# Performance work log

Hardware: AMD Instinct MI355X
Metric: run time of the kernel (lower is better)

Reference implementation:

```python
import jax, jax.numpy as jnp
import numpy as np


def _layernorm(x, g, b, eps=1e-5):
    mu = jnp.mean(x, axis=-1, keepdims=True)
    var = jnp.var(x, axis=-1, keepdims=True)
    return (x - mu) * jax.lax.rsqrt(var + eps) * g + b


def _forward(x_real, x_imag, dt, conv_w, conv_b, spec_re, spec_im, lam_re, lam_im,
             dt_param, sigma, noise_r, noise_i, ln_g, ln_b, W1, b1, w2, b2,
             Jg_W, Jg_b, Rg_W, Rg_b):
    B, T, C, H, W = x_real.shape
    x = x_real + 1j * x_imag  # complex field [B,T,C,H,W]

    # ---- spatial mixer: 3x3 conv applied to real/imag parts (linear op) ----
    def conv(z):
        z2 = z.reshape(B * T, C, H, W)
        y = jax.lax.conv_general_dilated(z2, conv_w, (1, 1), 'SAME',
                                         dimension_numbers=('NCHW', 'OIHW', 'NCHW'))
        return (y + conv_b[None, :, None, None]).reshape(B, T, C, H, W)
    x = x + (conv(x.real) + 1j * conv(x.imag))

    # ---- spectral mixer: pointwise complex filter in FFT domain ----
    Xf = jnp.fft.fft2(x, axes=(-2, -1), norm='ortho')
    filt = (spec_re + 1j * spec_im)[None, None]  # [1,1,C,H,W]
    x = x + jnp.fft.ifft2(Xf * filt, axes=(-2, -1), norm='ortho')

    # ---- metriplectic propagator: diagonal SSM scan in rfft2 space ----
    dt_eff = dt * jax.nn.softplus(dt_param)          # [C]
    dt_scalar = dt_eff.mean()
    xs = jnp.concatenate([x.real, x.imag], axis=0)   # [2B,T,C,H,W]; B_out=2B
    u = jnp.fft.rfft2(xs, axes=(-2, -1), norm='ortho')  # [2B,T,C,H,Wf]
    lam = -jax.nn.softplus(lam_re) + 1j * lam_im     # stable poles, [C]
    A = jnp.exp(lam * dt_eff.astype(jnp.complex64))  # [C]
    A = jnp.broadcast_to(A[None, None, :, None, None], u.shape)

    def comb(e1, e2):  # first-order linear recurrence h_t = a_t h_{t-1} + u_t
        a1, u1 = e1
        a2, u2 = e2
        return (a1 * a2, a2 * u1 + u2)
    _, h = jax.lax.associative_scan(comb, (A, u), axis=1)

    xt = jnp.fft.irfft2(h, s=(H, W), axes=(-2, -1), norm='ortho')  # [2B,T,C,H,W] real
    x_temporal = xt[:B] + 1j * xt[B:]

    noise = (noise_r + 1j * noise_i) * sigma * jnp.sqrt(dt_scalar)
    x = x + x_temporal + noise

    # ---- Port-Hamiltonian layer on real||imag channel concat ----
    xp = jnp.transpose(x, (0, 1, 3, 4, 2))                  # [B,T,H,W,C]
    xc = jnp.concatenate([xp.real, xp.imag], axis=-1)       # [B,T,H,W,2C]
    D = 2 * C
    x_in = _layernorm(xc, ln_g, ln_b)
    # grads of potential H = sum(MLP(x_in)) wrt x_in
    pot = lambda z: (jax.nn.silu(z @ W1 + b1) @ w2 + b2).sum()
    grads = jax.grad(pot)(x_in)
    M = (x_in @ Jg_W + Jg_b).reshape(*xc.shape[:-1], D, D)
    Jm = M - jnp.swapaxes(M, -1, -2)
    P = (x_in @ Rg_W + Rg_b).reshape(*xc.shape[:-1], D, D)
    R = jnp.einsum('...ki,...kj->...ij', P, P) + 1e-4 * jnp.eye(D, dtype=xc.dtype)
    update = jnp.einsum('...ij,...j->...i', Jm - R, grads)
    x_ph = xc + update * dt_scalar

    # output: [B,T,2C,H,W]; real half = out.real, imag half = out.imag
    return jnp.transpose(x_ph, (0, 1, 4, 2, 3))


def setup_inputs() -> dict:
    key = jax.random.key(0)
    ks = jax.random.split(key, 16)
    B, T, C, H, W = 2, 8, 16, 64, 64
    D = 2 * C
    hid = D * 4
    f32 = jnp.float32
    rn = lambda k, s, sc=1.0: jax.random.normal(k, s, f32) * sc
    return dict(
        x_real=rn(ks[0], (B, T, C, H, W)),
        x_imag=rn(ks[1], (B, T, C, H, W)),
        dt=jnp.asarray(0.1, f32),
        conv_w=rn(ks[2], (C, C, 3, 3), 0.05),
        conv_b=jnp.zeros((C,), f32),
        spec_re=rn(ks[3], (C, H, W), 0.1),
        spec_im=rn(ks[4], (C, H, W), 0.1),
        lam_re=rn(ks[5], (C,)),
        lam_im=rn(ks[6], (C,)),
        dt_param=rn(ks[7], (C,)),
        sigma=jnp.asarray(0.01, f32),
        noise_r=rn(ks[8], (B, T, C, H, W)),
        noise_i=rn(ks[9], (B, T, C, H, W)),
        ln_g=jnp.ones((D,), f32),
        ln_b=jnp.zeros((D,), f32),
        W1=rn(ks[10], (D, hid), 0.1),
        b1=jnp.zeros((hid,), f32),
        w2=rn(ks[11], (hid,), 0.1),
        b2=jnp.asarray(0.0, f32),
        Jg_W=rn(ks[12], (D, D * D), 0.02),
        Jg_b=jnp.zeros((D * D,), f32),
        Rg_W=rn(ks[13], (D, D * D), 0.02),
        Rg_b=jnp.zeros((D * D,), f32),
    )


def reference(x_real, x_imag, dt, conv_w, conv_b, spec_re, spec_im, lam_re, lam_im,
              dt_param, sigma, noise_r, noise_i, ln_g, ln_b, W1, b1, w2, b2,
              Jg_W, Jg_b, Rg_W, Rg_b):
    return _forward(x_real, x_imag, dt, conv_w, conv_b, spec_re, spec_im, lam_re,
                    lam_im, dt_param, sigma, noise_r, noise_i, ln_g, ln_b, W1, b1,
                    w2, b2, Jg_W, Jg_b, Rg_W, Rg_b)
```

## Files before the change

kernel.cpp:

```cpp
#include <hip/hip_runtime.h>
#include <math.h>
#include <utility>

#define Bb 2
#define Tt 8
#define Cc 16
#define Hh 64
#define Ww 64
#define Dd 32
#define HID 128
#define NPIX 4096
#define NIMG 256

typedef unsigned short ushort_t;
typedef unsigned int uint_t;
typedef __attribute__((ext_vector_type(8))) short short8;
typedef __attribute__((ext_vector_type(4))) float f32x4;
union U16 { uint4 u; short8 s; };

__device__ __forceinline__ float sp_f(float x) {
    return (x > 20.f) ? x : log1pf(expf(x));
}

__device__ __forceinline__ ushort_t f2bf(float f) {
    uint_t u = __float_as_uint(f);
    uint_t r = (u + 0x7fffu + ((u >> 16) & 1u)) >> 16;
    return (ushort_t)r;
}
__device__ __forceinline__ float bf2f(ushort_t h) { return __uint_as_float(((uint_t)h) << 16); }

__device__ __forceinline__ uint_t packbf(float hi, float lo) {
    return __builtin_amdgcn_perm(__float_as_uint(hi), __float_as_uint(lo), 0x07060302u);
}
__device__ __forceinline__ uint4 synth8(const float* gf, float xs) {
    uint4 r;
    r.x = packbf(gf[1] * xs, gf[0] * xs);
    r.y = packbf(gf[3] * xs, gf[2] * xs);
    r.z = packbf(gf[5] * xs, gf[4] * xs);
    r.w = packbf(gf[7] * xs, gf[6] * xs);
    return r;
}
__device__ __forceinline__ void expand8(uint4 v, float* f) {
    f[0] = __uint_as_float(v.x << 16); f[1] = __uint_as_float(v.x & 0xffff0000u);
    f[2] = __uint_as_float(v.y << 16); f[3] = __uint_as_float(v.y & 0xffff0000u);
    f[4] = __uint_as_float(v.z << 16); f[5] = __uint_as_float(v.z & 0xffff0000u);
    f[6] = __uint_as_float(v.w << 16); f[7] = __uint_as_float(v.w & 0xffff0000u);
}

template <typename F, int... Is>
__device__ __forceinline__ void unroll_impl(F&& f, std::integer_sequence<int, Is...>) {
    (f(std::integral_constant<int, Is>{}), ...);
}
template <int N, typename F>
__device__ __forceinline__ void cunroll(F&& f) {
    unroll_impl(f, std::make_integer_sequence<int, N>{});
}

#define MFMA16(a, b, c) __builtin_amdgcn_mfma_f32_16x16x32_bf16((a), (b), (c), 0, 0, 0)

struct cpx { float r, i; };
__device__ __forceinline__ cpx cadd(cpx a, cpx b) { return {a.r + b.r, a.i + b.i}; }
__device__ __forceinline__ cpx csub(cpx a, cpx b) { return {a.r - b.r, a.i - b.i}; }
__device__ __forceinline__ cpx cmulw(cpx a, float wr, float wi) {
    return {a.r * wr - a.i * wi, a.r * wi + a.i * wr};
}
template<int S>
__device__ __forceinline__ cpx cmulSi(cpx a) {
    return {-(float)S * a.i, (float)S * a.r};
}
template<int S>
__device__ __forceinline__ void dft8(cpx* y) {
    const float C = 0.70710678118654752f;
    cpx t0 = cadd(y[0], y[4]), t1 = csub(y[0], y[4]);
    cpx t2 = cadd(y[2], y[6]), t3 = csub(y[2], y[6]);
    cpx e0 = cadd(t0, t2), e2 = csub(t0, t2);
    cpx t3i = cmulSi<S>(t3);
    cpx e1 = cadd(t1, t3i), e3 = csub(t1, t3i);
    cpx u0 = cadd(y[1], y[5]), u1 = csub(y[1], y[5]);
    cpx u2 = cadd(y[3], y[7]), u3 = csub(y[3], y[7]);
    cpx o0 = cadd(u0, u2), o2 = csub(u0, u2);
    cpx u3i = cmulSi<S>(u3);
    cpx o1 = cadd(u1, u3i), o3 = csub(u1, u3i);
    o1 = cmulw(o1, C, (float)S * C);
    o2 = cmulSi<S>(o2);
    o3 = cmulw(o3, -C, (float)S * C);
    y[0] = cadd(e0, o0); y[4] = csub(e0, o0);
    y[1] = cadd(e1, o1); y[5] = csub(e1, o1);
    y[2] = cadd(e2, o2); y[6] = csub(e2, o2);
    y[3] = cadd(e3, o3); y[7] = csub(e3, o3);
}

template<int S>
__device__ __forceinline__ void fft2d_r8(float* reM, float* imM,
                                         const float* twr, const float* twi, int tid) {
    int j = tid & 63, g = tid >> 6;
    {
        cpx y[8];
        #pragma unroll
        for (int n1 = 0; n1 < 8; ++n1) {
            int a = j * 65 + n1 * 8 + g;
            y[n1] = {reM[a], imM[a]};
        }
        dft8<S>(y);
        #pragma unroll
        for (int k1 = 0; k1 < 8; ++k1) {
            int m = (g * k1) & 63;
            cpx b = cmulw(y[k1], twr[m], twi[m]);
            int a = j * 65 + k1 * 8 + g;
            reM[a] = b.r; imM[a] = b.i;
        }
    }
    __syncthreads();
    {
        cpx y[8];
        #pragma unroll
        for (int n2 = 0; n2 < 8; ++n2) {
            int a = j * 65 + g * 8 + n2;
            y[n2] = {reM[a], imM[a]};
        }
        dft8<S>(y);
        __syncthreads();
        #pragma unroll
        for (int k2 = 0; k2 < 8; ++k2) {
            int a = j * 65 + g + k2 * 8;
            reM[a] = y[k2].r; imM[a] = y[k2].i;
        }
    }
    __syncthreads();
    {
        cpx y[8];
        #pragma unroll
        for (int n1 = 0; n1 < 8; ++n1) {
            int a = (n1 * 8 + g) * 65 + j;
            y[n1] = {reM[a], imM[a]};
        }
        dft8<S>(y);
        #pragma unroll
        for (int k1 = 0; k1 < 8; ++k1) {
            int m = (g * k1) & 63;
            cpx b = cmulw(y[k1], twr[m], twi[m]);
            int a = (k1 * 8 + g) * 65 + j;
            reM[a] = b.r; imM[a] = b.i;
        }
    }
    __syncthreads();
    {
        cpx y[8];
        #pragma unroll
        for (int n2 = 0; n2 < 8; ++n2) {
            int a = (g * 8 + n2) * 65 + j;
            y[n2] = {reM[a], imM[a]};
        }
        dft8<S>(y);
        __syncthreads();
        #pragma unroll
        for (int k2 = 0; k2 < 8; ++k2) {
            int a = (g + k2 * 8) * 65 + j;
            reM[a] = y[k2].r; imM[a] = y[k2].i;
        }
    }
    __syncthreads();
}

__global__ __launch_bounds__(256)
void k_conv(const float* __restrict__ xr, const float* __restrict__ xi,
            const float* __restrict__ cw, const float* __restrict__ cb,
            float2* __restrict__ x1,
            const float* __restrict__ JW, const float* __restrict__ Jb,
            const float* __restrict__ RW, const float* __restrict__ Rb,
            const float* __restrict__ W1, const float* __restrict__ dtp,
            const float* __restrict__ dt_param,
            ushort_t* __restrict__ B1f, ushort_t* __restrict__ B2f,
            ushort_t* __restrict__ w1n, ushort_t* __restrict__ w1t,
            float* __restrict__ dts_out) {
    __shared__ float sre[Cc][18][18];
    __shared__ float sim[Cc][18][18];
    __shared__ float swt[8 * 16 * 12];
    __shared__ float sb[8];
    int tid = threadIdx.x;
    if (blockIdx.x >= 512) {
        const int N1 = 33 * 2048, N2 = 33 * 1024, N3 = 4096;
        int i = (blockIdx.x - 512) * 256 + tid;
        for (; i < N1 + N2 + N3; i += 40 * 256) {
            if (i < N1) {
                int s = i / 2048; int r = i % 2048;
                int ch = r >> 9; int lane = (r >> 3) & 63; int e = i & 7;
                int n = ch * 16 + (lane & 15);
                int k = s * 32 + ((lane >> 4) << 3) + e;
                float v;
                if (k < 1024) {
                    int d = k >> 5, rr = k & 31;
                    if (n < 32) v = JW[d * 1024 + n * 32 + rr] - JW[d * 1024 + rr * 32 + n];
                    else        v = RW[d * 1024 + (n - 32) * 32 + rr];
                } else {
                    int rr = k - 1024;
                    if (n < 32) v = Jb[n * 32 + rr] - Jb[rr * 32 + n];
                    else        v = Rb[(n - 32) * 32 + rr];
                }
                B1f[i] = f2bf(v);
            } else if (i < N1 + N2) {
                int i2 = i - N1;
                int s = i2 / 1024; int r = i2 % 1024;
                int ch = r >> 9; int lane = (r >> 3) & 63; int e = i2 & 7;
                int n = ch * 16 + (lane & 15);
                int k = s * 32 + ((lane >> 4) << 3) + e;
                float v;
                if (k < 1024) {
                    int d = k >> 5, kk = k & 31;
                    v = RW[d * 1024 + kk * 32 + n];
                } else {
                    v = Rb[(k - 1024) * 32 + n];
                }
                B2f[i2] = f2bf(v);
            } else {
                int i3 = i - N1 - N2;
                int d = i3 >> 7, h = i3 & 127;
                ushort_t v = f2bf(W1[i3]);
                w1n[i3] = v;
                w1t[h * 32 + d] = v;
            }
        }
        if (blockIdx.x == 512 && tid == 0) {
            float s = 0.f;
            for (int c = 0; c < Cc; ++c) s += sp_f(dt_param[c]);
            dts_out[0] = dtp[0] * s * (1.f / Cc);
        }
        return;
    }
    int blk = blockIdx.x;
    int bt = blk >> 5;
    int sub = blk & 31;
    int tile = sub >> 1, cohalf = sub & 1;
    int ty0 = (tile >> 2) * 16, tx0 = (tile & 3) * 16;
    for (int i = tid; i < 8 * 16 * 9; i += 256) {
        int g = i / 9, k = i % 9;
        swt[g * 12 + k] = cw[cohalf * 8 * 144 + i];
    }
    if (tid < 8) sb[tid] = cb[cohalf * 8 + tid];
    for (int i = tid; i < Cc * 18 * 18; i += 256) {
        int ci = i / 324; int r = i % 324; int y = r / 18, x = r % 18;
        int gy = ty0 + y - 1, gx = tx0 + x - 1;
        float vr = 0.f, vi = 0.f;
        if (gy >= 0 && gy < Hh && gx >= 0 && gx < Ww) {
            int gidx = (bt * Cc + ci) * NPIX + gy * Ww + gx;
            vr = xr[gidx]; vi = xi[gidx];
        }
        sre[ci][y][x] = vr; sim[ci][y][x] = vi;
    }
    __syncthreads();
    int py = tid >> 4, px = tid & 15;
    int gy = ty0 + py, gx = tx0 + px;
    float ar[8], ai[8];
    #pragma unroll
    for (int oc = 0; oc < 8; ++oc) {
        int cg = cohalf * 8 + oc;
        ar[oc] = sre[cg][py + 1][px + 1] + sb[oc];
        ai[oc] = sim[cg][py + 1][px + 1] + sb[oc];
    }
    for (int ci = 0; ci < Cc; ++ci) {
        float nr[9], ni[9];
        #pragma unroll
        for (int dy = 0; dy < 3; ++dy)
            #pragma unroll
            for (int dx = 0; dx < 3; ++dx) {
                nr[dy * 3 + dx] = sre[ci][py + dy][px + dx];
                ni[dy * 3 + dx] = sim[ci][py + dy][px + dx];
            }
        #pragma unroll
        for (int oc = 0; oc < 8; ++oc) {
            const float* wp = &swt[(oc * 16 + ci) * 12];
            float4 w0 = *(const float4*)&wp[0];
            float4 w1 = *(const float4*)&wp[4];
            float w8 = wp[8];
            ar[oc] += w0.x * nr[0] + w0.y * nr[1] + w0.z * nr[2]
                    + w0.w * nr[3] + w1.x * nr[4] + w1.y * nr[5]
                    + w1.z * nr[6] + w1.w * nr[7] + w8 * nr[8];
            ai[oc] += w0.x * ni[0] + w0.y * ni[1] + w0.z * ni[2]
                    + w0.w * ni[3] + w1.x * ni[4] + w1.y * ni[5]
                    + w1.z * ni[6] + w1.w * ni[7] + w8 * ni[8];
        }
    }
    #pragma unroll
    for (int oc = 0; oc < 8; ++oc)
        x1[(bt * Cc + cohalf * 8 + oc) * NPIX + gy * Ww + gx] = make_float2(ar[oc], ai[oc]);
}

__global__ __launch_bounds__(512)
void k_fft_fwd(const float2* __restrict__ x1,
               const float* __restrict__ spec_re, const float* __restrict__ spec_im,
               float2* __restrict__ X2f) {
    int img = blockIdx.x;
    int c = img % Cc;
    int tid = threadIdx.x;
    __shared__ float re[64 * 65], im[64 * 65];
    __shared__ float twr[64], twi[64];
    if (tid < 64) {
        float ang = -0.098174770424681038798f * (float)tid;
        twr[tid] = cosf(ang); twi[tid] = sinf(ang);
    }
    const float2* src = x1 + (size_t)img * NPIX;
    for (int idx = tid; idx < NPIX; idx += 512) {
        int h = idx >> 6, w = idx & 63;
        float2 v = src[idx];
        re[h * 65 + w] = v.x; im[h * 65 + w] = v.y;
    }
    __syncthreads();
    fft2d_r8<-1>(re, im, twr, twi, tid);
    const float* fr = spec_re + c * NPIX;
    const float* fi = spec_im + c * NPIX;
    float2* dst = X2f + (size_t)img * NPIX;
    for (int idx = tid; idx < NPIX; idx += 512) {
        int h = idx >> 6, w = idx & 63;
        float xr_ = re[h * 65 + w], xi_ = im[h * 65 + w];
        float gr = 1.f + fr[idx], gi = fi[idx];
        dst[idx] = make_float2(xr_ * gr - xi_ * gi, xi_ * gr + xr_ * gi);
    }
}

__global__ __launch_bounds__(256)
void k_scan2(const float2* __restrict__ Z,
             const float* __restrict__ lam_re, const float* __restrict__ lam_im,
             const float* __restrict__ dt_param, const float* __restrict__ dtp,
             float2* __restrict__ S) {
    int id = blockIdx.x * 256 + threadIdx.x;
    int w = id & 63;
    int c = (id >> 12) & 15;
    int b = id >> 16;
    float dte = dtp[0] * sp_f(dt_param[c]);
    float ea = expf(-sp_f(lam_re[c]) * dte);
    float ph = lam_im[c] * dte;
    float Ar = ea * cosf(ph), Ai = ea * sinf(ph);
    if (w > 32) Ai = -Ai;
    bool sc = (w == 0) || (w == 32);
    int pix = id & (NPIX - 1);
    int base = (b * Tt * Cc + c) * NPIX + pix;
    float s1r = 0.f, s1i = 0.f, s2r = 0.f, s2i = 0.f;
    #pragma unroll
    for (int t = 0; t < Tt; ++t) {
        int idx = base + t * (Cc * NPIX);
        float2 zv = Z[idx];
        float nr = Ar * s1r - Ai * s1i + zv.x;
        float ni = Ar * s1i + Ai * s1r + zv.y;
        s1r = nr; s1i = ni;
        float zr, zi;
        if (sc) {
            nr = Ar * s2r + Ai * s2i + zv.x;
            ni = Ar * s2i - Ai * s2r + zv.y;
            s2r = nr; s2i = ni;
            zr = 0.5f * (s1r + s2r); zi = 0.5f * (s1i + s2i);
        } else { zr = s1r; zi = s1i; }
        S[idx] = make_float2(zv.x + zr, zv.y + zi);
    }
}

__global__ __launch_bounds__(512)
void k_fft_inv(const float2* __restrict__ Sp,
               const float* __restrict__ noise_r, const float* __restrict__ noise_i,
               const float* __restrict__ sigma_p, const float* __restrict__ dts_p,
               float2* __restrict__ xf) {
    int img = blockIdx.x; int tid = threadIdx.x;
    __shared__ float re[64 * 65], im[64 * 65];
    __shared__ float twr[64], twi[64];
    if (tid < 64) {
        float ang = 0.098174770424681038798f * (float)tid;
        twr[tid] = cosf(ang); twi[tid] = sinf(ang);
    }
    const float2* src = Sp + (size_t)img * NPIX;
    for (int idx = tid; idx < NPIX; idx += 512) {
        int h = idx >> 6, w = idx & 63;
        float2 v = src[idx];
        re[h * 65 + w] = v.x; im[h * 65 + w] = v.y;
    }
    __syncthreads();
    fft2d_r8<1>(re, im, twr, twi, tid);
    float ns = sigma_p[0] * sqrtf(dts_p[0]);
    const float inv = 1.f / 4096.f;
    float2* dst = xf + (size_t)img * NPIX;
    const float* nr = noise_r + (size_t)img * NPIX;
    const float* ni = noise_i + (size_t)img * NPIX;
    for (int idx = tid; idx < NPIX; idx += 512) {
        int h = idx >> 6, w = idx & 63;
        dst[idx] = make_float2(re[h * 65 + w] * inv + ns * nr[idx],
                               im[h * 65 + w] * inv + ns * ni[idx]);
    }
}

__global__ __launch_bounds__(256, 2)
void k_ph(const float2* __restrict__ field,
          const float* __restrict__ ln_g, const float* __restrict__ ln_b,
          const float* __restrict__ b1, const float* __restrict__ w2,
          const ushort_t* __restrict__ w1n, const ushort_t* __restrict__ w1t,
          const ushort_t* __restrict__ B1f, const ushort_t* __restrict__ B2f,
          const float* __restrict__ dts_p,
          float* __restrict__ out) {
    __shared__ ushort_t xin_s[128 * 40];
    __shared__ ushort_t g_s[128 * 40];
    __shared__ ushort_t pg_s[128 * 40];
    __shared__ ushort_t A_s[128 * 136] __attribute__((aligned(16)));

    int tid = threadIdx.x;
    int bt = blockIdx.x >> 5;
    int pix0 = (blockIdx.x & 31) << 7;

    int p = tid & 127, half = tid >> 7;
    const float2* fbase = field + ((size_t)bt * 16) * NPIX + pix0 + p;
    float2 xv[8];
    float s1 = 0.f, s2 = 0.f;
    #pragma unroll
    for (int j = 0; j < 8; ++j) {
        xv[j] = fbase[(half * 8 + j) * NPIX];
        s1 += xv[j].x + xv[j].y;
        s2 += xv[j].x * xv[j].x + xv[j].y * xv[j].y;
    }
    float2* red = (float2*)A_s;
    red[p * 2 + half] = make_float2(s1, s2);
    __syncthreads();
    float2 r0 = red[p * 2], r1 = red[p * 2 + 1];
    float mu = (r0.x + r1.x) * 0.03125f;
    float var = (r0.y + r1.y) * 0.03125f - mu * mu;
    float rs = rsqrtf(var + 1e-5f);
    #pragma unroll
    for (int j = 0; j < 8; ++j) {
        int cf = half * 8 + j;
        xin_s[p * 40 + cf]      = f2bf((xv[j].x - mu) * rs * ln_g[cf] + ln_b[cf]);
        xin_s[p * 40 + cf + 16] = f2bf((xv[j].y - mu) * rs * ln_g[cf + 16] + ln_b[cf + 16]);
    }
    __syncthreads();

    int lane = tid & 63, wv = tid >> 6;
    int quad = lane >> 4, l15 = lane & 15;
    const f32x4 zero4 = {0.f, 0.f, 0.f, 0.f};
    int m0 = wv * 32;

    f32x4 zacc[2][8];
    #pragma unroll
    for (int mt = 0; mt < 2; ++mt)
        #pragma unroll
        for (int nt = 0; nt < 8; ++nt) zacc[mt][nt] = zero4;
    U16 az[2];
    #pragma unroll
    for (int mt = 0; mt < 2; ++mt)
        az[mt].u = *(const uint4*)&xin_s[(m0 + mt * 16 + l15) * 40 + quad * 8];
    #pragma unroll
    for (int nt = 0; nt < 8; ++nt) {
        U16 bz;
        bz.u = *(const uint4*)&w1t[(nt * 16 + l15) * 32 + quad * 8];
        zacc[0][nt] = MFMA16(az[0].s, bz.s, zacc[0][nt]);
        zacc[1][nt] = MFMA16(az[1].s, bz.s, zacc[1][nt]);
    }
    #pragma unroll
    for (int nt = 0; nt < 8; ++nt) {
        int col = nt * 16 + l15;
        float b1v = b1[col], w2v = w2[col];
        #pragma unroll
        for (int mt = 0; mt < 2; ++mt) {
            #pragma unroll
            for (int r = 0; r < 4; ++r) {
                int row = m0 + mt * 16 + quad * 4 + r;
                float z = zacc[mt][nt][r] + b1v;
                float s = 1.f / (1.f + expf(-z));
                float t = s * (1.f + z * (1.f - s)) * w2v;
                A_s[row * 136 + col] = f2bf(t);
            }
        }
    }
    __syncthreads();

    f32x4 gacc[2][2];
    #pragma unroll
    for (int mt = 0; mt < 2; ++mt)
        #pragma unroll
        for (int nt = 0; nt < 2; ++nt) gacc[mt][nt] = zero4;
    #pragma unroll
    for (int q = 0; q < 4; ++q) {
        U16 ag[2];
        #pragma unroll
        for (int mt = 0; mt < 2; ++mt)
            ag[mt].u = *(const uint4*)&A_s[(m0 + mt * 16 + l15) * 136 + q * 32 + quad * 8];
        #pragma unroll
        for (int nt = 0; nt < 2; ++nt) {
            U16 bg;
            bg.u = *(const uint4*)&w1n[(nt * 16 + l15) * 128 + q * 32 + quad * 8];
            gacc[0][nt] = MFMA16(ag[0].s, bg.s, gacc[0][nt]);
            gacc[1][nt] = MFMA16(ag[1].s, bg.s, gacc[1][nt]);
        }
    }
    #pragma unroll
    for (int mt = 0; mt < 2; ++mt)
        #pragma unroll
        for (int nt = 0; nt < 2; ++nt)
            #pragma unroll
            for (int r = 0; r < 4; ++r)
                g_s[(m0 + mt * 16 + quad * 4 + r) * 40 + nt * 16 + l15] = f2bf(gacc[mt][nt][r]);
    __syncthreads();

    const ushort_t* xr0 = &xin_s[(m0 + l15) * 40];
    const ushort_t* xr1 = &xin_s[(m0 + 16 + l15) * 40];
    uint4 gvp0 = *(const uint4*)&g_s[(m0 + l15) * 40 + quad * 8];
    uint4 gvp1 = *(const uint4*)&g_s[(m0 + 16 + l15) * 40 + quad * 8];
    float gf0[8], gf1[8];
    expand8(gvp0, gf0);
    expand8(gvp1, gf1);
    const uint4* B1v = (const uint4*)B1f;
    const uint4* B2v = (const uint4*)B2f;

    uint4 br[2][4];
    #pragma unroll
    for (int pf = 0; pf < 2; ++pf)
        #pragma unroll
        for (int ch = 0; ch < 4; ++ch)
            br[pf][ch] = B1v[(pf * 4 + ch) * 64 + lane];
    f32x4 acc1[4][2];
    #pragma unroll
    for (int ch = 0; ch < 4; ++ch) { acc1[ch][0] = zero4; acc1[ch][1] = zero4; }
    cunroll<33>([&](auto Sc) {
        constexpr int s = Sc.value;
        constexpr int cur = s & 1;
        U16 a0, a1;
        if constexpr (s < 32) {
            float x0 = bf2f(xr0[s]);
            float x1 = bf2f(xr1[s]);
            a0.u = synth8(gf0, x0);
            a1.u = synth8(gf1, x1);
        } else {
            a0.u = gvp0; a1.u = gvp1;
        }
        #pragma unroll
        for (int ch = 0; ch < 4; ++ch) {
            U16 b; b.u = br[cur][ch];
            acc1[ch][0] = MFMA16(a0.s, b.s, acc1[ch][0]);
            acc1[ch][1] = MFMA16(a1.s, b.s, acc1[ch][1]);
        }
        if constexpr (s + 2 < 33) {
            #pragma unroll
            for (int ch = 0; ch < 4; ++ch)
                br[cur][ch] = B1v[((s + 2) * 4 + ch) * 64 + lane];
        }
    });
    #pragma unroll
    for (int mt = 0; mt < 2; ++mt)
        #pragma unroll
        for (int c2 = 0; c2 < 2; ++c2)
            #pragma unroll
            for (int r = 0; r < 4; ++r)
                pg_s[(m0 + mt * 16 + quad * 4 + r) * 40 + c2 * 16 + l15] =
                    f2bf(acc1[2 + c2][mt][r]);
    __syncthreads();

    uint4 pgp0 = *(const uint4*)&pg_s[(m0 + l15) * 40 + quad * 8];
    uint4 pgp1 = *(const uint4*)&pg_s[(m0 + 16 + l15) * 40 + quad * 8];
    float pgf0[8], pgf1[8];
    expand8(pgp0, pgf0);
    expand8(pgp1, pgf1);
    uint4 br2[2][2];
    #pragma unroll
    for (int pf = 0; pf < 2; ++pf) {
        br2[pf][0] = B2v[(pf * 2 + 0) * 64 + lane];
        br2[pf][1] = B2v[(pf * 2 + 1) * 64 + lane];
    }
    f32x4 acc2[2][2];
    acc2[0][0] = zero4; acc2[0][1] = zero4; acc2[1][0] = zero4; acc2[1][1] = zero4;
    cunroll<33>([&](auto Sc) {
        constexpr int s = Sc.value;
        constexpr int cur = s & 1;
        U16 a0, a1;
        if constexpr (s < 32) {
            float x0 = bf2f(xr0[s]);
            float x1 = bf2f(xr1[s]);
            a0.u = synth8(pgf0, x0);
            a1.u = synth8(pgf1, x1);
        } else {
            a0.u = pgp0; a1.u = pgp1;
        }
        #pragma unroll
        for (int ch = 0; ch < 2; ++ch) {
            U16 b; b.u = br2[cur][ch];
            acc2[ch][0] = MFMA16(a0.s, b.s, acc2[ch][0]);
            acc2[ch][1] = MFMA16(a1.s, b.s, acc2[ch][1]);
        }
        if constexpr (s + 2 < 33) {
            br2[cur][0] = B2v[((s + 2) * 2 + 0) * 64 + lane];
            br2[cur][1] = B2v[((s + 2) * 2 + 1) * 64 + lane];
        }
    });

    __syncthreads();
    float* upd = (float*)A_s;
    #pragma unroll
    for (int mt = 0; mt < 2; ++mt) {
        #pragma unroll
        for (int c2 = 0; c2 < 2; ++c2) {
            int col = c2 * 16 + l15;
            #pragma unroll
            for (int r = 0; r < 4; ++r) {
                int row = m0 + mt * 16 + quad * 4 + r;
                float gval = bf2f(g_s[row * 40 + col]);
                upd[row * 33 + col] = acc1[c2][mt][r] - acc2[c2][mt][r] - 1e-4f * gval;
            }
        }
    }
    __syncthreads();
    float dts = dts_p[0];
    #pragma unroll
    for (int cc = 0; cc < 16; ++cc) {
        int c = half * 16 + cc;
        float2 v = fbase[cc * NPIX];
        float xcv = half ? v.y : v.x;
        out[((size_t)bt * 32 + c) * NPIX + pix0 + p] = xcv + dts * upd[p * 33 + c];
    }
}

extern "C" void kernel_launch(void* const* d_in, const int* in_sizes, int n_in,
                              void* d_out, int out_size, void* d_ws, size_t ws_size,
                              hipStream_t stream) {
    const float* x_real   = (const float*)d_in[0];
    const float* x_imag   = (const float*)d_in[1];
    const float* dt       = (const float*)d_in[2];
    const float* conv_w   = (const float*)d_in[3];
    const float* conv_b   = (const float*)d_in[4];
    const float* spec_re  = (const float*)d_in[5];
    const float* spec_im  = (const float*)d_in[6];
    const float* lam_re   = (const float*)d_in[7];
    const float* lam_im   = (const float*)d_in[8];
    const float* dt_param = (const float*)d_in[9];
    const float* sigma    = (const float*)d_in[10];
    const float* noise_r  = (const float*)d_in[11];
    const float* noise_i  = (const float*)d_in[12];
    const float* ln_g     = (const float*)d_in[13];
    const float* ln_b     = (const float*)d_in[14];
    const float* W1       = (const float*)d_in[15];
    const float* b1       = (const float*)d_in[16];
    const float* w2       = (const float*)d_in[17];
    const float* Jg_W     = (const float*)d_in[19];
    const float* Jg_b     = (const float*)d_in[20];
    const float* Rg_W     = (const float*)d_in[21];
    const float* Rg_b     = (const float*)d_in[22];

    float2* wsA = (float2*)d_ws;
    float2* wsB = wsA + 1048576;
    float2* wsS = wsB + 1048576;

    ushort_t* B1f = (ushort_t*)(wsS + 1048576);
    ushort_t* B2f = B1f + 33 * 2048;
    ushort_t* w1n = B2f + 33 * 1024;
    ushort_t* w1t = w1n + 4096;
    float*    dts = (float*)(w1t + 4096);

    k_conv<<<552, 256, 0, stream>>>(x_real, x_imag, conv_w, conv_b, wsA,
                                    Jg_W, Jg_b, Rg_W, Rg_b, W1, dt, dt_param,
                                    B1f, B2f, w1n, w1t, dts);
    k_fft_fwd<<<NIMG, 512, 0, stream>>>(wsA, spec_re, spec_im, wsB);
    k_scan2<<<512, 256, 0, stream>>>(wsB, lam_re, lam_im, dt_param, dt, wsS);
    k_fft_inv<<<NIMG, 512, 0, stream>>>(wsS, noise_r, noise_i, sigma, dts, wsA);
    k_ph<<<512, 256, 0, stream>>>(wsA, ln_g, ln_b, b1, w2, w1n, w1t, B1f, B2f, dts,
                                  (float*)d_out);
}
```

Before: 182.3 us.

## Fuse temporal scan into inverse FFT kernel via direct convolution over time

Removes the separate scan kernel and its intermediate buffer. Each inverse-FFT block now builds its timestep's scan output directly as a weighted sum of earlier frequency-domain frames, using powers of the pole, before running the inverse FFT. This saves one launch and one full write and read of the intermediate field, but a block at timestep t reads t+1 frames, so total reads rise to roughly 4.5x the field across the blocks.

```diff
diff --git a/kernel.cpp b/kernel.cpp
--- a/kernel.cpp
+++ b/kernel.cpp
@@ -317,59 +317,53 @@
     }
 }
 
-__global__ __launch_bounds__(256)
-void k_scan2(const float2* __restrict__ Z,
-             const float* __restrict__ lam_re, const float* __restrict__ lam_im,
-             const float* __restrict__ dt_param, const float* __restrict__ dtp,
-             float2* __restrict__ S) {
-    int id = blockIdx.x * 256 + threadIdx.x;
-    int w = id & 63;
-    int c = (id >> 12) & 15;
-    int b = id >> 16;
-    float dte = dtp[0] * sp_f(dt_param[c]);
-    float ea = expf(-sp_f(lam_re[c]) * dte);
-    float ph = lam_im[c] * dte;
-    float Ar = ea * cosf(ph), Ai = ea * sinf(ph);
-    if (w > 32) Ai = -Ai;
-    bool sc = (w == 0) || (w == 32);
-    int pix = id & (NPIX - 1);
-    int base = (b * Tt * Cc + c) * NPIX + pix;
-    float s1r = 0.f, s1i = 0.f, s2r = 0.f, s2i = 0.f;
-    #pragma unroll
-    for (int t = 0; t < Tt; ++t) {
-        int idx = base + t * (Cc * NPIX);
-        float2 zv = Z[idx];
-        float nr = Ar * s1r - Ai * s1i + zv.x;
-        float ni = Ar * s1i + Ai * s1r + zv.y;
-        s1r = nr; s1i = ni;
-        float zr, zi;
-        if (sc) {
-            nr = Ar * s2r + Ai * s2i + zv.x;
-            ni = Ar * s2i - Ai * s2r + zv.y;
-            s2r = nr; s2i = ni;
-            zr = 0.5f * (s1r + s2r); zi = 0.5f * (s1i + s2i);
-        } else { zr = s1r; zi = s1i; }
-        S[idx] = make_float2(zv.x + zr, zv.y + zi);
-    }
-}
-
 __global__ __launch_bounds__(512)
-void k_fft_inv(const float2* __restrict__ Sp,
+void k_fft_inv(const float2* __restrict__ Z,
+               const float* __restrict__ lam_re, const float* __restrict__ lam_im,
+               const float* __restrict__ dt_param, const float* __restrict__ dtp,
                const float* __restrict__ noise_r, const float* __restrict__ noise_i,
                const float* __restrict__ sigma_p, const float* __restrict__ dts_p,
                float2* __restrict__ xf) {
     int img = blockIdx.x; int tid = threadIdx.x;
+    int b = img >> 7, t = (img >> 4) & 7, c = img & 15;
     __shared__ float re[64 * 65], im[64 * 65];
     __shared__ float twr[64], twi[64];
     if (tid < 64) {
         float ang = 0.098174770424681038798f * (float)tid;
         twr[tid] = cosf(ang); twi[tid] = sinf(ang);
     }
-    const float2* src = Sp + (size_t)img * NPIX;
-    for (int idx = tid; idx < NPIX; idx += 512) {
-        int h = idx >> 6, w = idx & 63;
-        float2 v = src[idx];
-        re[h * 65 + w] = v.x; im[h * 65 + w] = v.y;
+    float dte = dtp[0] * sp_f(dt_param[c]);
+    float ea = expf(-sp_f(lam_re[c]) * dte);
+    float ph = lam_im[c] * dte;
+    float A1r = ea * cosf(ph), A1i = ea * sinf(ph);
+    int w = tid & 63;
+    float sgn = (w == 0 || w == 32) ? 0.f : ((w > 32) ? -1.f : 1.f);
+
+    float accr[8], acci[8];
+    #pragma unroll
+    for (int j = 0; j < 8; ++j) { accr[j] = 0.f; acci[j] = 0.f; }
+    float Ar = 1.f, Ai = 0.f;
+    for (int k = 0; k <= t; ++k) {
+        const float2* Zk = Z + ((size_t)((b * Tt + (t - k)) * Cc + c)) * NPIX;
+        float cr = Ar, ci = sgn * Ai;
+        #pragma unroll
+        for (int j = 0; j < 8; ++j) {
+            float2 z = Zk[tid + j * 512];
+            accr[j] += cr * z.x - ci * z.y;
+            acci[j] += cr * z.y + ci * z.x;
+        }
+        float nr = Ar * A1r - Ai * A1i;
+        Ai = Ar * A1i + Ai * A1r;
+        Ar = nr;
+    }
+    const float2* Zt = Z + (size_t)img * NPIX;
+    #pragma unroll
+    for (int j = 0; j < 8; ++j) {
+        int idx = tid + j * 512;
+        int h = idx >> 6;
+        float2 z = Zt[idx];
+        re[h * 65 + w] = z.x + accr[j];
+        im[h * 65 + w] = z.y + acci[j];
     }
     __syncthreads();
     fft2d_r8<1>(re, im, twr, twi, tid);
@@ -379,9 +373,9 @@
     const float* nr = noise_r + (size_t)img * NPIX;
     const float* ni = noise_i + (size_t)img * NPIX;
     for (int idx = tid; idx < NPIX; idx += 512) {
-        int h = idx >> 6, w = idx & 63;
-        dst[idx] = make_float2(re[h * 65 + w] * inv + ns * nr[idx],
-                               im[h * 65 + w] * inv + ns * ni[idx]);
+        int h = idx >> 6, ww = idx & 63;
+        dst[idx] = make_float2(re[h * 65 + ww] * inv + ns * nr[idx],
+                               im[h * 65 + ww] * inv + ns * ni[idx]);
     }
 }
 
@@ -638,9 +632,8 @@
 
     float2* wsA = (float2*)d_ws;
     float2* wsB = wsA + 1048576;
-    float2* wsS = wsB + 1048576;
-
-    ushort_t* B1f = (ushort_t*)(wsS + 1048576);
+
+    ushort_t* B1f = (ushort_t*)(wsB + 1048576);
     ushort_t* B2f = B1f + 33 * 2048;
     ushort_t* w1n = B2f + 33 * 1024;
     ushort_t* w1t = w1n + 4096;
@@ -650,8 +643,8 @@
                                     Jg_W, Jg_b, Rg_W, Rg_b, W1, dt, dt_param,
                                     B1f, B2f, w1n, w1t, dts);
     k_fft_fwd<<<NIMG, 512, 0, stream>>>(wsA, spec_re, spec_im, wsB);
-    k_scan2<<<512, 256, 0, stream>>>(wsB, lam_re, lam_im, dt_param, dt, wsS);
-    k_fft_inv<<<NIMG, 512, 0, stream>>>(wsS, noise_r, noise_i, sigma, dts, wsA);
+    k_fft_inv<<<NIMG, 512, 0, stream>>>(wsB, lam_re, lam_im, dt_param, dt,
+                                        noise_r, noise_i, sigma, dts, wsA);
     k_ph<<<512, 256, 0, stream>>>(wsA, ln_g, ln_b, b1, w2, w1n, w1t, B1f, B2f, dts,
                                   (float*)d_out);
 }
```

Result: no change. 182.6 us (+0.2%).
